# Kernel optimization log

Measured on AMD Instinct MI355X. Metric: run time of the kernel, lower is better.

The kernel has to match this reference:

```python
import jax, jax.numpy as jnp
import numpy as np

B, D, Nh, L = 8, 128, 8, 1024
Dk = D // Nh  # 16
Dv = D // Nh  # 16

def _xavier(key, shape):
    # nn.init.xavier_normal_ on a 3D tensor treats dim0 as fan irrelevant:
    # fan_in = shape[-1]*1, fan_out = shape[-2]*1 for >=2D; receptive field = prod(shape[2:])? For 3D torch uses
    # fan_in = shape[1]*shape[2]? We just need same distribution family; use std from last two dims.
    fan_in, fan_out = shape[-1], shape[-2]
    std = float(np.sqrt(2.0 / (fan_in + fan_out)))
    return jax.random.normal(key, shape, dtype=jnp.float32) * std

def setup_inputs() -> dict:
    key = jax.random.key(0)
    kx, kq, kk, kv, ko = jax.random.split(key, 5)
    x = jax.random.normal(kx, (B, D, L), dtype=jnp.float32)
    Wq = _xavier(kq, (Nh, B, Dk, D))
    Wk = _xavier(kk, (Nh, B, Dk, D))
    Wv = _xavier(kv, (Nh, B, Dv, D))
    Wo = _xavier(ko, (B, Dv * Nh, D))
    return {"x": x, "Wq": Wq, "Wk": Wk, "Wv": Wv, "Wo": Wo}

def reference(x, Wq, Wk, Wv, Wo):
    scale = 1.0 / np.sqrt(Dk)
    # Project all heads at once: [Nh,B,Dk,D] x [B,D,L] -> [B,Nh,Dk,L]
    Q = jnp.einsum('hbkd,bdl->bhkl', Wq, x)
    K = jnp.einsum('hbkd,bdl->bhkl', Wk, x)
    V = jnp.einsum('hbvd,bdl->bhvl', Wv, x)
    # scores[b,h,i,j] = sum_k Q[b,h,k,i] * K[b,h,k,j]
    scores = jnp.einsum('bhki,bhkj->bhij', Q, K) * scale
    # original softmaxes over dim=1 of [B,L,L] -> the i (Q-length) axis
    attn = jax.nn.softmax(scores, axis=2)
    # head[b,h,v,j] = sum_i V[b,h,v,i] * attn[b,h,i,j]
    head = jnp.einsum('bhvi,bhij->bhvj', V, attn)
    # concat heads along channel dim (order matches torch.cat over head list)
    head = head.reshape(B, Nh * Dv, L)
    # Wo [B, Nh*Dv, D] bmm head [B, D(=Nh*Dv), L] -> [B, Nh*Dv, L]
    out = jnp.einsum('bod,bdl->bol', Wo, head)
    return out
```

## Files before the change

kernel.cpp:

```cpp
#include <hip/hip_runtime.h>
#include <hip/hip_bf16.h>

#define B_ 8
#define D_ 128
#define NH 8
#define L_ 1024
#define DK 16

typedef __attribute__((ext_vector_type(4))) short s4;
typedef __attribute__((ext_vector_type(4))) float f4;

static __device__ __forceinline__ unsigned short f2bf(float f) {
    __hip_bfloat16 h = __float2bfloat16(f);
    return *reinterpret_cast<unsigned short*>(&h);
}
static __device__ __forceinline__ unsigned pack2(float a, float b) {
    return (unsigned)f2bf(a) | ((unsigned)f2bf(b) << 16);
}
static __device__ __forceinline__ s4 pack4(float a, float b, float c, float d) {
    union { unsigned u[2]; s4 v; } un;
    un.u[0] = pack2(a, b);
    un.u[1] = pack2(c, d);
    return un.v;
}

static __device__ __forceinline__ float fexp2(float x) {
#if __has_builtin(__builtin_amdgcn_exp2f)
    return __builtin_amdgcn_exp2f(x);
#else
    float r; asm("v_exp_f32 %0, %1" : "=v"(r) : "v"(x)); return r;
#endif
}

#if __has_builtin(__builtin_amdgcn_mfma_f32_16x16x16_bf16)
#define MFMA16(a, b, c) __builtin_amdgcn_mfma_f32_16x16x16_bf16(a, b, c, 0, 0, 0)
#elif __has_builtin(__builtin_amdgcn_mfma_f32_16x16x16bf16_1k)
#define MFMA16(a, b, c) __builtin_amdgcn_mfma_f32_16x16x16bf16_1k(a, b, c, 0, 0, 0)
#else
static __device__ __forceinline__ f4 mfma16_asm(s4 a, s4 b, f4 c) {
    f4 d;
    asm volatile("v_mfma_f32_16x16x16_bf16 %0, %1, %2, %3"
                 : "=&v"(d) : "v"(a), "v"(b), "v"(c));
    return d;
}
#define MFMA16(a, b, c) mfma16_asm(a, b, c)
#endif

__global__ __launch_bounds__(256)
void proj_kernel(const float* __restrict__ x,
                 const float* __restrict__ Wq,
                 const float* __restrict__ Wk,
                 const float* __restrict__ Wv,
                 unsigned short* __restrict__ Qt,
                 unsigned short* __restrict__ Kt,
                 unsigned short* __restrict__ Vt) {
    const int lane = threadIdx.x & 63;
    const int wv   = threadIdx.x >> 6;
    const int m = lane & 15, q = lane >> 4;
    const int bh = blockIdx.y, b = bh >> 3, h = bh & 7;
    const int n0 = (blockIdx.x * 4 + wv) * 16;

    const size_t wrow_off = ((size_t)((h * B_ + b) * DK + m)) * D_;
    const float* Wqr = Wq + wrow_off;
    const float* Wkr = Wk + wrow_off;
    const float* Wvr = Wv + wrow_off;
    const float* xb = x + (size_t)b * D_ * L_ + n0 + m;

    f4 aQ = {0.f, 0.f, 0.f, 0.f}, aK = {0.f, 0.f, 0.f, 0.f}, aV = {0.f, 0.f, 0.f, 0.f};
#pragma unroll
    for (int kb = 0; kb < 8; ++kb) {
        const int k4 = kb * 16 + q * 4;

        const float* xc = xb + (size_t)k4 * L_;
        float b0 = xc[0], b1 = xc[L_], b2 = xc[2 * L_], b3 = xc[3 * L_];
        s4 bf = pack4(b0, b1, b2, b3);

        float4 wq = *(const float4*)(Wqr + k4);
        float4 wk = *(const float4*)(Wkr + k4);
        float4 wv4 = *(const float4*)(Wvr + k4);
        s4 fq = pack4(wq.x, wq.y, wq.z, wq.w);
        s4 fk = pack4(wk.x, wk.y, wk.z, wk.w);
        s4 fv = pack4(wv4.x, wv4.y, wv4.z, wv4.w);

        aQ = MFMA16(fq, bf, aQ);
        aK = MFMA16(fk, bf, aK);
        aV = MFMA16(fv, bf, aV);
    }

    uint2 uq;
    uq.x = pack2(aQ[0], aQ[1]);
    uq.y = pack2(aQ[2], aQ[3]);
    *(uint2*)(Qt + ((size_t)bh * L_ + n0 + m) * DK + q * 4) = uq;

    const float sc = 0.25f * 1.4426950408889634f;
    uint2 uk;
    uk.x = pack2(aK[0] * sc, aK[1] * sc);
    uk.y = pack2(aK[2] * sc, aK[3] * sc);
    *(uint2*)(Kt + ((size_t)bh * L_ + n0 + m) * DK + q * 4) = uk;

    unsigned short* vp = Vt + ((size_t)bh * DK + q * 4) * L_ + n0 + m;
    vp[0]      = f2bf(aV[0]); vp[L_]     = f2bf(aV[1]);
    vp[2 * L_] = f2bf(aV[2]); vp[3 * L_] = f2bf(aV[3]);
}

__global__ __launch_bounds__(1024)
void attn_out_kernel(const unsigned short* __restrict__ Qt,
                     const unsigned short* __restrict__ Kt,
                     const unsigned short* __restrict__ Vt,
                     const float* __restrict__ Wo,
                     float* __restrict__ out) {
    const int lane = threadIdx.x & 63;
    const int wid  = threadIdx.x >> 6;
    const int m = lane & 15, q = lane >> 4;
    const int b    = blockIdx.y;
    const int jblk = blockIdx.x * 16;

    const int h     = wid & 7;
    const int ihalf = wid >> 3;
    const int bh    = b * NH + h;

    __shared__ unsigned short hls[16][132];
    __shared__ float red[8][64][8];

    s4 bk = *(const s4*)(Kt + ((size_t)bh * L_ + jblk + m) * DK + q * 4);

    f4 O = {0.f, 0.f, 0.f, 0.f};
    float ls = 0.f;
    const unsigned short* qbase = Qt + (size_t)bh * L_ * DK + q * 4
                                     + (size_t)(ihalf * (L_ / 2)) * DK;
    const unsigned short* vbase = Vt + ((size_t)bh * DK + m) * L_ + q * 4
                                     + ihalf * (L_ / 2);

#pragma unroll 4
    for (int i0 = 0; i0 < L_ / 2; i0 += 16) {
        s4 aq = *(const s4*)(qbase + (size_t)(i0 + m) * DK);
        s4 av = *(const s4*)(vbase + i0);

        f4 z = {0.f, 0.f, 0.f, 0.f};
        f4 S = MFMA16(aq, bk, z);

        float p0 = fexp2(S[0]), p1 = fexp2(S[1]);
        float p2 = fexp2(S[2]), p3 = fexp2(S[3]);
        ls += (p0 + p1) + (p2 + p3);

        s4 pb;
        pb[0] = (short)f2bf(p0); pb[1] = (short)f2bf(p1);
        pb[2] = (short)f2bf(p2); pb[3] = (short)f2bf(p3);

        O = MFMA16(av, pb, O);
    }

    ls += __shfl_xor(ls, 16, 64);
    ls += __shfl_xor(ls, 32, 64);

    if (ihalf) {
        float* r = red[h][lane];
        *(f4*)(r) = O;
        r[4] = ls;
    }
    __syncthreads();
    if (!ihalf) {
        const float* r = red[h][lane];
        f4 P = *(const f4*)(r);
        O += P;
        const float inv = 1.f / (ls + r[4]);

        uint2 o0;
        o0.x = pack2(O[0] * inv, O[1] * inv);
        o0.y = pack2(O[2] * inv, O[3] * inv);
        *(uint2*)&hls[m][h * 16 + q * 4] = o0;
    }
    __syncthreads();

    if (wid < 8) {
        const int o0 = wid * 16;
        const float* Wrow = Wo + ((size_t)b * D_ + o0 + m) * D_;

        f4 acc = {0.f, 0.f, 0.f, 0.f};
#pragma unroll
        for (int kb = 0; kb < 8; ++kb) {
            const int k4 = kb * 16 + q * 4;
            float4 wf = *(const float4*)(Wrow + k4);
            s4 a  = pack4(wf.x, wf.y, wf.z, wf.w);
            s4 bb = *(const s4*)&hls[m][k4];
            acc = MFMA16(a, bb, acc);
        }

        float* op = out + ((size_t)b * D_ + o0 + q * 4) * L_ + jblk + m;
        op[0]      = acc[0]; op[L_]     = acc[1];
        op[2 * L_] = acc[2]; op[3 * L_] = acc[3];
    }
}

extern "C" void kernel_launch(void* const* d_in, const int* in_sizes, int n_in,
                              void* d_out, int out_size, void* d_ws, size_t ws_size,
                              hipStream_t stream) {
    const float* x  = (const float*)d_in[0];
    const float* Wq = (const float*)d_in[1];
    const float* Wk = (const float*)d_in[2];
    const float* Wv = (const float*)d_in[3];
    const float* Wo = (const float*)d_in[4];
    float* out = (float*)d_out;

    const size_t SEG = (size_t)B_ * NH * DK * L_;
    unsigned short* Qt = (unsigned short*)d_ws;
    unsigned short* Kt = Qt + SEG;
    unsigned short* Vt = Kt + SEG;

    proj_kernel<<<dim3(16, B_ * NH), 256, 0, stream>>>(x, Wq, Wk, Wv, Qt, Kt, Vt);
    attn_out_kernel<<<dim3(64, B_), 1024, 0, stream>>>(Qt, Kt, Vt, Wo, out);
}
```

Baseline: 119.2 us.

## Split attention and output projection; stage per-head Q and V in LDS

New measurement: 99.59 us. 1.2x faster.

```diff
diff --git a/kernel.cpp b/kernel.cpp
--- a/kernel.cpp
+++ b/kernel.cpp
@@ -104,92 +104,100 @@
 }
 
 __global__ __launch_bounds__(1024)
-void attn_out_kernel(const unsigned short* __restrict__ Qt,
-                     const unsigned short* __restrict__ Kt,
-                     const unsigned short* __restrict__ Vt,
-                     const float* __restrict__ Wo,
-                     float* __restrict__ out) {
+void attn_kernel(const unsigned short* __restrict__ Qt,
+                 const unsigned short* __restrict__ Kt,
+                 const unsigned short* __restrict__ Vt,
+                 unsigned short* __restrict__ Ht) {
+    const int tid  = threadIdx.x;
+    const int lane = tid & 63;
+    const int wid  = tid >> 6;
+    const int m = lane & 15, q = lane >> 4;
+    const int jg = blockIdx.x, bh = blockIdx.y;
+
+    __shared__ s4 Qf[64 * 64];
+    __shared__ s4 Vf[64 * 64];
+
+    const unsigned short* Qg = Qt + (size_t)bh * L_ * DK;
+    const unsigned short* Vg = Vt + (size_t)bh * DK * L_;
+#pragma unroll
+    for (int c = 0; c < 4; ++c) {
+        const int e  = c * 1024 + tid;
+        const int it = e >> 6;
+        const int em = e & 15;
+        const int eq = (e >> 4) & 3;
+        Qf[e] = *(const s4*)(Qg + (size_t)(it * 16 + em) * DK + eq * 4);
+        Vf[e] = *(const s4*)(Vg + (size_t)em * L_ + it * 16 + eq * 4);
+    }
+
+    const int j0 = jg * 256 + wid * 16;
+    s4 bk = *(const s4*)(Kt + ((size_t)bh * L_ + j0 + m) * DK + q * 4);
+
+    __syncthreads();
+
+    f4 O = {0.f, 0.f, 0.f, 0.f};
+    float ls = 0.f;
+#pragma unroll 8
+    for (int it = 0; it < 64; ++it) {
+        s4 aq = Qf[it * 64 + lane];
+        s4 av = Vf[it * 64 + lane];
+
+        f4 z = {0.f, 0.f, 0.f, 0.f};
+        f4 S = MFMA16(aq, bk, z);
+
+        float p0 = fexp2(S[0]), p1 = fexp2(S[1]);
+        float p2 = fexp2(S[2]), p3 = fexp2(S[3]);
+        ls += (p0 + p1) + (p2 + p3);
+
+        s4 pb;
+        pb[0] = (short)f2bf(p0); pb[1] = (short)f2bf(p1);
+        pb[2] = (short)f2bf(p2); pb[3] = (short)f2bf(p3);
+
+        O = MFMA16(av, pb, O);
+    }
+
+    ls += __shfl_xor(ls, 16, 64);
+    ls += __shfl_xor(ls, 32, 64);
+    const float inv = 1.f / ls;
+
+    unsigned short* hp = Ht + ((size_t)bh * DK + q * 4) * L_ + j0 + m;
+    hp[0]      = f2bf(O[0] * inv); hp[L_]     = f2bf(O[1] * inv);
+    hp[2 * L_] = f2bf(O[2] * inv); hp[3 * L_] = f2bf(O[3] * inv);
+}
+
+__global__ __launch_bounds__(1024)
+void outproj_kernel(const unsigned short* __restrict__ Ht,
+                    const float* __restrict__ Wo,
+                    float* __restrict__ out) {
     const int lane = threadIdx.x & 63;
     const int wid  = threadIdx.x >> 6;
     const int m = lane & 15, q = lane >> 4;
-    const int b    = blockIdx.y;
-    const int jblk = blockIdx.x * 16;
-
-    const int h     = wid & 7;
-    const int ihalf = wid >> 3;
-    const int bh    = b * NH + h;
-
-    __shared__ unsigned short hls[16][132];
-    __shared__ float red[8][64][8];
-
-    s4 bk = *(const s4*)(Kt + ((size_t)bh * L_ + jblk + m) * DK + q * 4);
-
-    f4 O = {0.f, 0.f, 0.f, 0.f};
-    float ls = 0.f;
-    const unsigned short* qbase = Qt + (size_t)bh * L_ * DK + q * 4
-                                     + (size_t)(ihalf * (L_ / 2)) * DK;
-    const unsigned short* vbase = Vt + ((size_t)bh * DK + m) * L_ + q * 4
-                                     + ihalf * (L_ / 2);
-
-#pragma unroll 4
-    for (int i0 = 0; i0 < L_ / 2; i0 += 16) {
-        s4 aq = *(const s4*)(qbase + (size_t)(i0 + m) * DK);
-        s4 av = *(const s4*)(vbase + i0);
-
-        f4 z = {0.f, 0.f, 0.f, 0.f};
-        f4 S = MFMA16(aq, bk, z);
-
-        float p0 = fexp2(S[0]), p1 = fexp2(S[1]);
-        float p2 = fexp2(S[2]), p3 = fexp2(S[3]);
-        ls += (p0 + p1) + (p2 + p3);
-
-        s4 pb;
-        pb[0] = (short)f2bf(p0); pb[1] = (short)f2bf(p1);
-        pb[2] = (short)f2bf(p2); pb[3] = (short)f2bf(p3);
-
-        O = MFMA16(av, pb, O);
-    }
-
-    ls += __shfl_xor(ls, 16, 64);
-    ls += __shfl_xor(ls, 32, 64);
-
-    if (ihalf) {
-        float* r = red[h][lane];
-        *(f4*)(r) = O;
-        r[4] = ls;
-    }
-    __syncthreads();
-    if (!ihalf) {
-        const float* r = red[h][lane];
-        f4 P = *(const f4*)(r);
-        O += P;
-        const float inv = 1.f / (ls + r[4]);
-
-        uint2 o0;
-        o0.x = pack2(O[0] * inv, O[1] * inv);
-        o0.y = pack2(O[2] * inv, O[3] * inv);
-        *(uint2*)&hls[m][h * 16 + q * 4] = o0;
-    }
-    __syncthreads();
-
-    if (wid < 8) {
-        const int o0 = wid * 16;
-        const float* Wrow = Wo + ((size_t)b * D_ + o0 + m) * D_;
-
-        f4 acc = {0.f, 0.f, 0.f, 0.f};
+    const int b = blockIdx.y;
+    const int oc = wid & 7, jt = wid >> 3;
+    const int j16 = blockIdx.x * 32 + jt * 16;
+    const int o0 = oc * 16;
+
+    const float* Wrow = Wo + ((size_t)b * D_ + o0 + m) * D_;
+    const unsigned short* Hb = Ht + (size_t)b * D_ * L_ + j16 + m;
+
+    f4 acc = {0.f, 0.f, 0.f, 0.f};
 #pragma unroll
-        for (int kb = 0; kb < 8; ++kb) {
-            const int k4 = kb * 16 + q * 4;
-            float4 wf = *(const float4*)(Wrow + k4);
-            s4 a  = pack4(wf.x, wf.y, wf.z, wf.w);
-            s4 bb = *(const s4*)&hls[m][k4];
-            acc = MFMA16(a, bb, acc);
-        }
-
-        float* op = out + ((size_t)b * D_ + o0 + q * 4) * L_ + jblk + m;
-        op[0]      = acc[0]; op[L_]     = acc[1];
-        op[2 * L_] = acc[2]; op[3 * L_] = acc[3];
-    }
+    for (int kb = 0; kb < 8; ++kb) {
+        const int k4 = kb * 16 + q * 4;
+        float4 wf = *(const float4*)(Wrow + k4);
+        s4 a = pack4(wf.x, wf.y, wf.z, wf.w);
+
+        const unsigned short* hp = Hb + (size_t)k4 * L_;
+        s4 bb;
+        bb[0] = (short)hp[0];
+        bb[1] = (short)hp[L_];
+        bb[2] = (short)hp[2 * L_];
+        bb[3] = (short)hp[3 * L_];
+        acc = MFMA16(a, bb, acc);
+    }
+
+    float* op = out + ((size_t)b * D_ + o0 + q * 4) * L_ + j16 + m;
+    op[0]      = acc[0]; op[L_]     = acc[1];
+    op[2 * L_] = acc[2]; op[3 * L_] = acc[3];
 }
 
 extern "C" void kernel_launch(void* const* d_in, const int* in_sizes, int n_in,
@@ -206,7 +214,9 @@
     unsigned short* Qt = (unsigned short*)d_ws;
     unsigned short* Kt = Qt + SEG;
     unsigned short* Vt = Kt + SEG;
+    unsigned short* Ht = Vt + SEG;
 
     proj_kernel<<<dim3(16, B_ * NH), 256, 0, stream>>>(x, Wq, Wk, Wv, Qt, Kt, Vt);
-    attn_out_kernel<<<dim3(64, B_), 1024, 0, stream>>>(Qt, Kt, Vt, Wo, out);
-}
+    attn_kernel<<<dim3(4, B_ * NH), 1024, 0, stream>>>(Qt, Kt, Vt, Ht);
+    outproj_kernel<<<dim3(32, B_), 1024, 0, stream>>>(Ht, Wo, out);
+}
```
